# Kernel tuning notes

Measured on AMD Instinct MI355X. Metric: run time of the kernel, lower is better.

## Reference

```python
import jax, jax.numpy as jnp
import numpy as np

B, LQ, NK, D, H, FF, NL = 32, 96, 2048, 384, 8, 1536, 6
DH = D // H
NFUT = 32
GOAL_S, GRASP_S = 2046, 2047  # goal=[2046,2047), grasp=[2047,2048) in k_cross and k_self


def rotary3d(xyz):
    # RotaryPositionEncoding3D: per-axis sinusoids, interleaved duplication, concat over x/y/z
    d3 = D // 3
    div = jnp.exp(jnp.arange(0, d3, 2, dtype=jnp.float32) * (-np.log(10000.0) / d3))  # [d3/2]
    ang = xyz[..., None] * div  # [B,N,3,d3/2]
    cos = jnp.repeat(jnp.cos(ang), 2, axis=-1)  # [B,N,3,d3] (f0,f0,f1,f1,...)
    sin = jnp.repeat(jnp.sin(ang), 2, axis=-1)
    b, n = xyz.shape[:2]
    return cos.reshape(b, n, D), sin.reshape(b, n, D)


def rope(x, cos, sin):
    x2 = jnp.stack([-x[..., 1::2], x[..., ::2]], axis=-1).reshape(x.shape)
    return x * cos + x2 * sin


def layernorm(x, g, b):
    m = jnp.mean(x, -1, keepdims=True)
    v = jnp.var(x, -1, keepdims=True)
    return (x - m) * jax.lax.rsqrt(v + 1e-5) * g + b


def attn_block(x, kv, qcos, qsin, kcos, ksin, t_feats, p):
    (aw, ab, wq_, bq_, wk_, bk_, wv_, bv_, wo_, bo_, g1, b1, fw1_, fb1_, fw2_, fb2_, g2, b2_) = p
    # AdaLN: time-conditioned scale/shift on the query stream
    mod = jax.nn.silu(t_feats) @ aw + ab  # [B,2D]
    scale, shift = jnp.split(mod, 2, axis=-1)
    xq = x * (1.0 + scale[:, None, :]) + shift[:, None, :]
    qp = rope(xq @ wq_ + bq_, qcos, qsin).reshape(B, -1, H, DH)
    kp = rope(kv @ wk_ + bk_, kcos, ksin).reshape(B, -1, H, DH)
    vp = (kv @ wv_ + bv_).reshape(B, -1, H, DH)
    att = jax.nn.softmax(jnp.einsum('bqhd,bkhd->bhqk', qp, kp) / np.sqrt(DH), axis=-1)
    o = jnp.einsum('bhqk,bkhd->bqhd', att, vp).reshape(B, -1, D) @ wo_ + bo_
    x = layernorm(x + o, g1, b1)  # post-norm (pre_norm=False), residual on un-modulated x
    f = jax.nn.relu(x @ fw1_ + fb1_) @ fw2_ + fb2_
    return layernorm(x + f, g2, b2_)


def mlp_head(x, w1, b1, w2, b2, w3, b3):
    h = jax.nn.relu(x @ w1 + b1)
    h = jax.nn.relu(h @ w2 + b2)
    return h @ w3 + b3


def _forward(q, k_cross, k_self, q_xyz, k_xyz, timesteps,
             t_w1, t_b1, t_w2, t_b2, type_emb,
             ada_w, ada_b, wq, bq, wk, bk, wv, bv, wo, bo,
             ln1_g, ln1_b, fw1, fb1, fw2, fb2, ln2_g, ln2_b,
             act_w1, act_b1, act_w2, act_b2, act_w3, act_b3,
             qf_w1, qf_b1, qf_w2, qf_b2, qf_w3, qf_b3,
             ob_w1, ob_b1, ob_w2, ob_b2, ob_w3, ob_b3):
    # SinusoidalPosEmb + MLP time embedding
    half = D // 2
    freqs = jnp.exp(jnp.arange(half, dtype=jnp.float32) * (-np.log(10000.0) / (half - 1)))
    a = timesteps[:, None] * freqs
    pe = jnp.concatenate([jnp.sin(a), jnp.cos(a)], axis=-1)
    t_feats = jax.nn.relu(pe @ t_w1 + t_b1) @ t_w2 + t_b2  # [B,D]

    qcos, qsin = rotary3d(q_xyz)
    kcos, ksin = rotary3d(k_xyz)
    scos = jnp.concatenate([kcos, qcos], axis=1)  # self layers: seq2_pos = cat(pcd, grasp)
    ssin = jnp.concatenate([ksin, qsin], axis=1)

    # type embeddings (conditions_only -> goal=id3, grasp=id4)
    kc = k_cross.at[:, GOAL_S:GOAL_S + 1].add(type_emb[3]).at[:, GRASP_S:GRASP_S + 1].add(type_emb[4])
    ksf = k_self.at[:, GOAL_S:GOAL_S + 1].add(type_emb[3]).at[:, GRASP_S:GRASP_S + 1].add(type_emb[4])

    x = q
    for i in range(NL):
        p = (ada_w[i], ada_b[i], wq[i], bq[i], wk[i], bk[i], wv[i], bv[i], wo[i], bo[i],
             ln1_g[i], ln1_b[i], fw1[i], fb1[i], fw2[i], fb2[i], ln2_g[i], ln2_b[i])
        if i < 2:  # cross_attn module (2 layers) over scene tokens
            x = attn_block(x, kc, qcos, qsin, kcos, ksin, t_feats, p)
        else:      # 4 shared attention layers over k_self
            x = attn_block(x, ksf, qcos, qsin, scos, ssin, t_feats, p)

    act = mlp_head(x[:, :NFUT], act_w1, act_b1, act_w2, act_b2, act_w3, act_b3)            # [B,32,31]
    qf = mlp_head(x[:, NFUT:2 * NFUT], qf_w1, qf_b1, qf_w2, qf_b2, qf_w3, qf_b3)           # [B,32,31]
    ob = mlp_head(x[:, 2 * NFUT:], ob_w1, ob_b1, ob_w2, ob_b2, ob_w3, ob_b3)               # [B,32,9]
    return jnp.concatenate([act, qf, ob], axis=-1)  # [B,32,71]


def setup_inputs():
    ks = iter(jax.random.split(jax.random.key(0), 80))
    def w(shape, s=0.02):
        return jax.random.normal(next(ks), shape, jnp.float32) * s
    inp = {
        'q': jax.random.normal(next(ks), (B, LQ, D), jnp.float32),
        'k_cross': jax.random.normal(next(ks), (B, NK, D), jnp.float32),
        'k_self': jax.random.normal(next(ks), (B, NK + LQ, D), jnp.float32),
        'q_xyz': jax.random.normal(next(ks), (B, LQ, 3), jnp.float32),
        'k_xyz': jax.random.normal(next(ks), (B, NK, 3), jnp.float32),
        'timesteps': jax.random.uniform(next(ks), (B,), jnp.float32) * 1000.0,
        't_w1': w((D, D)), 't_b1': jnp.zeros((D,)), 't_w2': w((D, D)), 't_b2': jnp.zeros((D,)),
        'type_emb': w((8, D)),
        'ada_w': w((NL, D, 2 * D)), 'ada_b': jnp.zeros((NL, 2 * D)),
        'wq': w((NL, D, D)), 'bq': jnp.zeros((NL, D)),
        'wk': w((NL, D, D)), 'bk': jnp.zeros((NL, D)),
        'wv': w((NL, D, D)), 'bv': jnp.zeros((NL, D)),
        'wo': w((NL, D, D)), 'bo': jnp.zeros((NL, D)),
        'ln1_g': jnp.ones((NL, D)), 'ln1_b': jnp.zeros((NL, D)),
        'fw1': w((NL, D, FF)), 'fb1': jnp.zeros((NL, FF)),
        'fw2': w((NL, FF, D)), 'fb2': jnp.zeros((NL, D)),
        'ln2_g': jnp.ones((NL, D)), 'ln2_b': jnp.zeros((NL, D)),
        'act_w1': w((D, D)), 'act_b1': jnp.zeros((D,)), 'act_w2': w((D, D)), 'act_b2': jnp.zeros((D,)),
        'act_w3': w((D, 31)), 'act_b3': jnp.zeros((31,)),
        'qf_w1': w((D, D)), 'qf_b1': jnp.zeros((D,)), 'qf_w2': w((D, D)), 'qf_b2': jnp.zeros((D,)),
        'qf_w3': w((D, 31)), 'qf_b3': jnp.zeros((31,)),
        'ob_w1': w((D, D)), 'ob_b1': jnp.zeros((D,)), 'ob_w2': w((D, D)), 'ob_b2': jnp.zeros((D,)),
        'ob_w3': w((D, 9)), 'ob_b3': jnp.zeros((9,)),
    }
    return inp


def reference(q, k_cross, k_self, q_xyz, k_xyz, timesteps,
              t_w1, t_b1, t_w2, t_b2, type_emb,
              ada_w, ada_b, wq, bq, wk, bk, wv, bv, wo, bo,
              ln1_g, ln1_b, fw1, fb1, fw2, fb2, ln2_g, ln2_b,
              act_w1, act_b1, act_w2, act_b2, act_w3, act_b3,
              qf_w1, qf_b1, qf_w2, qf_b2, qf_w3, qf_b3,
              ob_w1, ob_b1, ob_w2, ob_b2, ob_w3, ob_b3):
    return _forward(q, k_cross, k_self, q_xyz, k_xyz, timesteps,
                    t_w1, t_b1, t_w2, t_b2, type_emb,
                    ada_w, ada_b, wq, bq, wk, bk, wv, bv, wo, bo,
                    ln1_g, ln1_b, fw1, fb1, fw2, fb2, ln2_g, ln2_b,
                    act_w1, act_b1, act_w2, act_b2, act_w3, act_b3,
                    qf_w1, qf_b1, qf_w2, qf_b2, qf_w3, qf_b3,
                    ob_w1, ob_b1, ob_w2, ob_b2, ob_w3, ob_b3)
```

## Files before the change

### kernel.cpp

```cpp
#include <hip/hip_runtime.h>
#include <hip/hip_fp16.h>

#define B_   32
#define LQ_  96
#define NK_  2048
#define D_   384
#define H_   8
#define DH_  48
#define FF_  1536
#define MQ_  (B_*LQ_)
#define SATT 8

typedef float  f32x4  __attribute__((ext_vector_type(4)));
typedef __bf16 bf16x8 __attribute__((ext_vector_type(8)));

__device__ __forceinline__ unsigned short f2bf(float f) {
  union { float f; unsigned u; } v; v.f = f;
  unsigned r = v.u + 0x7fffu + ((v.u >> 16) & 1u);
  return (unsigned short)(r >> 16);
}

__device__ __forceinline__ void ld_g2l(const unsigned short* g, unsigned short* l) {
  __builtin_amdgcn_global_load_lds(
      (const __attribute__((address_space(1))) void*)g,
      (__attribute__((address_space(3))) void*)l, 16, 0, 0);
}

__global__ void time_embed_kernel(const float* __restrict__ ts,
                                  const float* __restrict__ w1, const float* __restrict__ b1,
                                  const float* __restrict__ w2, const float* __restrict__ b2,
                                  float* __restrict__ s_out) {
  int b = blockIdx.x, d = threadIdx.x;
  __shared__ float pe[384];
  __shared__ float h1[384];
  float t = ts[b];
  int dd = (d < 192) ? d : d - 192;
  float f = expf((float)dd * (-9.210340371976184f / 191.0f));
  float ang = t * f;
  pe[d] = (d < 192) ? sinf(ang) : cosf(ang);
  __syncthreads();
  float acc = b1[d];
  for (int k = 0; k < 384; ++k) acc += pe[k] * w1[k * 384 + d];
  h1[d] = fmaxf(acc, 0.f);
  __syncthreads();
  acc = b2[d];
  for (int k = 0; k < 384; ++k) acc += h1[k] * w2[k * 384 + d];
  s_out[b * 384 + d] = acc / (1.f + expf(-acc));
}

__global__ void adaln_mod_kernel(const float* __restrict__ s,
                                 const float* __restrict__ aw, const float* __restrict__ ab,
                                 float* __restrict__ mod) {
  int b = blockIdx.x, l = blockIdx.y, c = threadIdx.x;
  __shared__ float ss[384];
  if (c < 384) ss[c] = s[b * 384 + c];
  __syncthreads();
  float acc = ab[l * 768 + c];
  const float* w = aw + (long)l * 384 * 768;
  for (int k = 0; k < 384; ++k) acc += ss[k] * w[k * 768 + c];
  mod[((long)l * 32 + b) * 768 + c] = acc;
}

__global__ void rope_pack_kernel(const float* __restrict__ xyz, __half2* __restrict__ cs,
                                 int total, int N, int ldn, int noff) {
  for (int i = blockIdx.x * blockDim.x + threadIdx.x; i < total;
       i += gridDim.x * blockDim.x) {
    int p = i % 192;
    int n = (i / 192) % N;
    int b = i / (192 * N);
    int a = p >> 6, j = p & 63;
    float div = __expf((float)j * (-9.210340371976184f / 64.0f));
    float ang = xyz[((long)b * N + n) * 3 + a] * div;
    float sv, cv;
    __sincosf(ang, &sv, &cv);
    cs[((long)b * ldn + noff + n) * 192 + p] = __floats2half2_rn(cv, sv);
  }
}

__global__ void cast_type_kernel(const float* __restrict__ in, const float* __restrict__ temb,
                                 unsigned short* __restrict__ out, long total, int N) {
  for (long i = blockIdx.x * (long)blockDim.x + threadIdx.x; i < total;
       i += (long)gridDim.x * blockDim.x) {
    int d = (int)(i % 384);
    int n = (int)((i / 384) % N);
    float v = in[i];
    if (n == 2046) v += temb[3 * 384 + d];
    else if (n == 2047) v += temb[4 * 384 + d];
    out[i] = f2bf(v);
  }
}

__global__ void wtrans_kernel(const float* __restrict__ in, unsigned short* __restrict__ out,
                              long total, int K, int N, int LDN, int noff) {
  for (long i = blockIdx.x * (long)blockDim.x + threadIdx.x; i < total;
       i += (long)gridDim.x * blockDim.x) {
    long l = i / ((long)K * N);
    long rem = i - l * (long)K * N;
    int n = (int)(rem / K);
    int k = (int)(rem % K);
    out[(l * LDN + noff + n) * K + k] = f2bf(in[l * (long)K * N + (long)k * N + n]);
  }
}

__global__ void modx_kernel(const float* __restrict__ x, const float* __restrict__ modl,
                            unsigned short* __restrict__ xq) {
  int i = blockIdx.x * blockDim.x + threadIdx.x;
  if (i >= MQ_ * D_) return;
  int d = i % 384;
  int b = (i / 384) / 96;
  float sc = modl[b * 768 + d];
  float sh = modl[b * 768 + 384 + d];
  xq[i] = f2bf(x[i] * (1.f + sc) + sh);
}

#define EPI_RELU   1
#define EPI_F32    2
#define EPI_ROPE_Q 3
#define EPI_KV     4

template <int EPI, int TM, int XT, int PERM>
__global__ __launch_bounds__(256)
void gemm_bt(const unsigned short* __restrict__ A, const unsigned short* __restrict__ Bt,
             const float* __restrict__ biasK, const float* __restrict__ biasV,
             void* __restrict__ Cout, void* __restrict__ Cout2,
             int Nt, int K, const __half2* __restrict__ cs, int tabOff, int nPerRow) {
  __shared__ __align__(16) unsigned short As[2][TM * 32];
  __shared__ __align__(16) unsigned short Bs[2][128 * 32];
  int tid = threadIdx.x, lane = tid & 63, wid = tid >> 6;
  int wm = (wid >> 1) * (TM / 2), wn = (wid & 1) * 64;
  int bx, byi;
  if (XT > 0) {
    int id = blockIdx.x;
    int xcd = id & 7, slot = id >> 3;
    bx = slot % XT;
    byi = (slot / XT) * 8 + xcd;
  } else {
    bx = blockIdx.x; byi = blockIdx.y;
  }
  int bn = bx * 128;
  long bm = (long)byi * TM;
  int r0 = tid >> 2;
  int cg = ((tid & 3) + (tid >> 3)) & 3;
  int c0 = cg * 8;
  long ar0 = bm + r0, ar1 = bm + 64 + r0;
  if (PERM) {
    ar0 = (ar0 >> 5) * 96 + tabOff + (ar0 & 31);
    ar1 = (ar1 >> 5) * 96 + tabOff + (ar1 & 31);
  }
  const unsigned short* gA0 = A + ar0 * K + c0;
  const unsigned short* gA1 = A + ar1 * K + c0;
  const unsigned short* gB0 = Bt + (long)(bn + r0) * K + c0;
  const unsigned short* gB1 = Bt + (long)(bn + 64 + r0) * K + c0;
  f32x4 acc[TM / 32][4] = {};
  int nk = K >> 5;
  int la = lane & 15, lg8 = lane >> 4;
  ld_g2l(gA0, &As[0][tid * 8]);
  if (TM == 128) ld_g2l(gA1, &As[0][2048 + tid * 8]);
  ld_g2l(gB0, &Bs[0][tid * 8]);
  ld_g2l(gB1, &Bs[0][2048 + tid * 8]);
  gA0 += 32; gA1 += 32; gB0 += 32; gB1 += 32;
  int offA[TM / 32], offB[4];
#pragma unroll
  for (int i = 0; i < TM / 32; ++i) {
    int row = wm + i * 16 + la;
    offA[i] = row * 32 + ((lg8 - (row >> 1)) & 3) * 8;
  }
#pragma unroll
  for (int j = 0; j < 4; ++j) {
    int row = wn + j * 16 + la;
    offB[j] = row * 32 + ((lg8 - (row >> 1)) & 3) * 8;
  }
  __syncthreads();
  for (int kc = 0; kc < nk; ++kc) {
    int cur = kc & 1;
    if (kc + 1 < nk) {
      int nxt = cur ^ 1;
      ld_g2l(gA0, &As[nxt][tid * 8]);
      if (TM == 128) ld_g2l(gA1, &As[nxt][2048 + tid * 8]);
      ld_g2l(gB0, &Bs[nxt][tid * 8]);
      ld_g2l(gB1, &Bs[nxt][2048 + tid * 8]);
      gA0 += 32; gA1 += 32; gB0 += 32; gB1 += 32;
    }
    bf16x8 af[TM / 32], bfr[4];
#pragma unroll
    for (int i = 0; i < TM / 32; ++i) af[i] = *(const bf16x8*)&As[cur][offA[i]];
#pragma unroll
    for (int j = 0; j < 4; ++j) bfr[j] = *(const bf16x8*)&Bs[cur][offB[j]];
#pragma unroll
    for (int i = 0; i < TM / 32; ++i)
#pragma unroll
      for (int j = 0; j < 4; ++j)
        acc[i][j] = __builtin_amdgcn_mfma_f32_16x16x32_bf16(af[i], bfr[j], acc[i][j], 0, 0, 0);
    __syncthreads();
  }
  int lr = lg8 * 4;
  const float SCALE = 0.14433756729740643f;
  bool isV = false;
  const float* bptr = biasK;
  if (EPI == EPI_KV) { isV = (bn >= 384); if (isV) bptr = biasV - 384; }
#pragma unroll
  for (int i = 0; i < TM / 32; ++i) {
#pragma unroll
    for (int r = 0; r < 4; ++r) {
      int row = (int)bm + wm + i * 16 + lr + r;
      int bb = 0, nn = 0; long ti = 0;
      if (EPI == EPI_ROPE_Q || EPI == EPI_KV) {
        bb = row / nPerRow;
        nn = row - bb * nPerRow;
        ti = ((long)bb * 2144 + tabOff + nn) * 192;
      }
#pragma unroll
      for (int j = 0; j < 4; ++j) {
        int col = bn + wn + j * 16 + la;
        float v = acc[i][j][r] + bptr[col];
        if (EPI == EPI_F32) {
          ((float*)Cout)[(long)row * Nt + col] = v;
        } else if (EPI == EPI_RELU) {
          ((unsigned short*)Cout)[(long)row * Nt + col] = f2bf(fmaxf(v, 0.f));
        } else if (EPI == EPI_KV && isV) {
          ((unsigned short*)Cout2)[(long)row * 384 + (col - 384)] = f2bf(v);
        } else {
          float pv = __shfl_xor(v, 1);
          int p = ((col >> 7) << 6) + ((col & 127) >> 1);
          __half2 hv = cs[ti + p];
          float cc = __low2float(hv), ssv = __high2float(hv);
          float o = (col & 1) ? (v * cc + pv * ssv) : (v * cc - pv * ssv);
          if (EPI == EPI_ROPE_Q) {
            ((unsigned short*)Cout)[(long)row * Nt + col] = f2bf(o * SCALE);
          } else {
            int h = col / 48, d = col - h * 48;
            ((unsigned short*)Cout)[((long)((bb << 3) + h) * nPerRow + nn) * 48 + d] = f2bf(o);
          }
        }
      }
    }
  }
}

__global__ __launch_bounds__(384)
void attn_part_kernel(const unsigned short* __restrict__ Q, const unsigned short* __restrict__ Kg,
                      const unsigned short* __restrict__ Vrm, float* __restrict__ Opart,
                      float* __restrict__ Lpart, int N, int S) {
  int h = blockIdx.x, b = blockIdx.y, s = blockIdx.z;
  int bh = b * 8 + h;
  int tid = threadIdx.x, lane = tid & 63, w = tid >> 6;
  __shared__ __align__(16) unsigned short Qs[96][64];
  __shared__ __align__(16) unsigned short Ks[32][72];
  __shared__ __align__(16) unsigned short Vst[64][40];
  __shared__ __align__(16) unsigned short Ps[6][16][40];
  const uint4 z4 = {0u, 0u, 0u, 0u};
  for (int e = tid; e < 576; e += 384) {
    int row = e / 6, g = e % 6;
    *(uint4*)&Qs[row][g * 8] = *(const uint4*)&Q[((long)b * 96 + row) * 384 + h * 48 + g * 8];
  }
  for (int e = tid; e < 192; e += 384) {
    int row = e >> 1, g = e & 1;
    *(uint4*)&Qs[row][48 + g * 8] = z4;
  }
  if (tid < 96) {
    int row = tid / 3, g = tid % 3;
    *(uint4*)&Ks[row][48 + g * 8] = z4;
  }
  if (tid < 75) *(uint4*)&Vst[49][0 + tid * 8] = z4;
  if (tid < 40) Vst[48][tid] = (tid < 32) ? (unsigned short)0x3F80 : (unsigned short)0;
  __syncthreads();
  int la = lane & 15, lg = (lane >> 4) * 8;
  bf16x8 qf0 = *(const bf16x8*)&Qs[w * 16 + la][lg];
  bf16x8 qf1 = *(const bf16x8*)&Qs[w * 16 + la][32 + lg];
  f32x4 of[4] = {};
  int ntile = N >> 5;
  int t0 = (s * ntile) / S, t1 = ((s + 1) * ntile) / S;
  int stt = (tid < 192) ? tid : tid - 192;
  int krow = stt / 6, kg = stt % 6;
  const uint4* gsrc = (tid < 192)
      ? (const uint4*)(Kg + ((long)bh * N + krow) * 48 + kg * 8)
      : (const uint4*)(Vrm + ((long)b * N + krow) * 384 + h * 48 + kg * 8);
  int tstep = (tid < 192) ? 192 : 1536;
  uint4 pref = gsrc[(long)t0 * tstep];
  for (int it = t0; it < t1; ++it) {
    if (tid < 192) {
      *(uint4*)&Ks[krow][kg * 8] = pref;
    } else {
      union { uint4 q; unsigned short u[8]; } t; t.q = pref;
#pragma unroll
      for (int e = 0; e < 8; ++e) Vst[kg * 8 + e][krow] = t.u[e];
    }
    __syncthreads();
    if (it + 1 < t1) pref = gsrc[(long)(it + 1) * tstep];
    f32x4 sc[2] = {};
#pragma unroll
    for (int ctile = 0; ctile < 2; ++ctile) {
      bf16x8 kf0 = *(const bf16x8*)&Ks[ctile * 16 + la][lg];
      bf16x8 kf1 = *(const bf16x8*)&Ks[ctile * 16 + la][32 + lg];
      sc[ctile] = __builtin_amdgcn_mfma_f32_16x16x32_bf16(qf0, kf0, sc[ctile], 0, 0, 0);
      sc[ctile] = __builtin_amdgcn_mfma_f32_16x16x32_bf16(qf1, kf1, sc[ctile], 0, 0, 0);
    }
    int prow = (lane >> 4) * 4;
#pragma unroll
    for (int ctile = 0; ctile < 2; ++ctile)
#pragma unroll
      for (int r = 0; r < 4; ++r)
        Ps[w][prow + r][ctile * 16 + la] = f2bf(__expf(sc[ctile][r]));
    __asm__ volatile("s_waitcnt lgkmcnt(0)" ::: "memory");
    bf16x8 pf = *(const bf16x8*)&Ps[w][la][lg];
#pragma unroll
    for (int dt = 0; dt < 4; ++dt) {
      bf16x8 vf = *(const bf16x8*)&Vst[dt * 16 + la][lg];
      of[dt] = __builtin_amdgcn_mfma_f32_16x16x32_bf16(pf, vf, of[dt], 0, 0, 0);
    }
    __syncthreads();
  }
  long base = ((long)s * 256 + bh) * 96;
#pragma unroll
  for (int r = 0; r < 4; ++r) {
    int qrow = w * 16 + (lane >> 4) * 4 + r;
    float L = __shfl(of[3][r], lane & 48);
#pragma unroll
    for (int dt = 0; dt < 3; ++dt)
      Opart[(base + qrow) * 48 + dt * 16 + la] = of[dt][r];
    if (la == 0) Lpart[base + qrow] = L;
  }
}

__global__ __launch_bounds__(384)
void attn_combine_kernel(const float* __restrict__ Opart, const float* __restrict__ Lpart,
                         unsigned short* __restrict__ O, int S) {
  int h = blockIdx.x, b = blockIdx.y;
  int bh = b * 8 + h;
  for (int e = threadIdx.x; e < 96 * 48; e += 384) {
    int q = e / 48, d = e % 48;
    float L = 0.f, acc = 0.f;
    for (int s = 0; s < S; ++s) {
      long ib = ((long)s * 256 + bh) * 96 + q;
      L += Lpart[ib];
      acc += Opart[ib * 48 + d];
    }
    O[((long)b * 96 + q) * 384 + h * 48 + d] = f2bf(acc / L);
  }
}

__global__ __launch_bounds__(128)
void ln_res_kernel(const float* __restrict__ xin, const float* __restrict__ delta,
                   const float* __restrict__ g, const float* __restrict__ bt,
                   const float* __restrict__ modl,
                   float* __restrict__ xout, unsigned short* __restrict__ xbf,
                   unsigned short* __restrict__ xqb) {
  int row = blockIdx.x, tid = threadIdx.x;
  __shared__ float red[128];
  float v[3];
#pragma unroll
  for (int i = 0; i < 3; ++i) {
    int d = tid + i * 128;
    v[i] = xin[(long)row * 384 + d] + delta[(long)row * 384 + d];
  }
  red[tid] = v[0] + v[1] + v[2];
  __syncthreads();
  for (int t = 64; t > 0; t >>= 1) { if (tid < t) red[tid] += red[tid + t]; __syncthreads(); }
  float mean = red[0] / 384.f;
  __syncthreads();
  float q = 0.f;
#pragma unroll
  for (int i = 0; i < 3; ++i) { float d0 = v[i] - mean; q += d0 * d0; }
  red[tid] = q;
  __syncthreads();
  for (int t = 64; t > 0; t >>= 1) { if (tid < t) red[tid] += red[tid + t]; __syncthreads(); }
  float rstd = rsqrtf(red[0] / 384.f + 1e-5f);
  int bb = row / 96;
#pragma unroll
  for (int i = 0; i < 3; ++i) {
    int d = tid + i * 128;
    float o = (v[i] - mean) * rstd * g[d] + bt[d];
    xout[(long)row * 384 + d] = o;
    xbf[(long)row * 384 + d] = f2bf(o);
    if (modl) {
      float sc = modl[bb * 768 + d];
      float sh = modl[bb * 768 + 384 + d];
      xqb[(long)row * 384 + d] = f2bf(o * (1.f + sc) + sh);
    }
  }
}

__global__ __launch_bounds__(64)
void rowgemm_bf(const unsigned short* __restrict__ A, const float* __restrict__ W,
                const float* __restrict__ bias, float* __restrict__ out,
                int Nc, int ooff) {
  int r = blockIdx.x, tid = threadIdx.x;
  __shared__ float as[384];
  for (int k = tid; k < 384; k += 64) {
    union { unsigned u; float f; } c; c.u = (unsigned)A[(long)r * 384 + k] << 16;
    as[k] = c.f;
  }
  __syncthreads();
  if (tid < Nc) {
    float acc = bias[tid];
    for (int k = 0; k < 384; ++k) acc += as[k] * W[k * Nc + tid];
    out[(long)r * 71 + ooff + tid] = acc;
  }
}

extern "C" void kernel_launch(void* const* d_in, const int* in_sizes, int n_in,
                              void* d_out, int out_size, void* d_ws, size_t ws_size,
                              hipStream_t stream) {
  const float* q_in    = (const float*)d_in[0];
  const float* k_cross = (const float*)d_in[1];
  const float* k_self  = (const float*)d_in[2];
  const float* q_xyz   = (const float*)d_in[3];
  const float* k_xyz   = (const float*)d_in[4];
  const float* tsteps  = (const float*)d_in[5];
  const float* t_w1 = (const float*)d_in[6];
  const float* t_b1 = (const float*)d_in[7];
  const float* t_w2 = (const float*)d_in[8];
  const float* t_b2 = (const float*)d_in[9];
  const float* type_emb = (const float*)d_in[10];
  const float* ada_w = (const float*)d_in[11];
  const float* ada_b = (const float*)d_in[12];
  const float* wq = (const float*)d_in[13]; const float* bq = (const float*)d_in[14];
  const float* wk = (const float*)d_in[15]; const float* bk = (const float*)d_in[16];
  const float* wv = (const float*)d_in[17]; const float* bv = (const float*)d_in[18];
  const float* wo = (const float*)d_in[19]; const float* bo = (const float*)d_in[20];
  const float* ln1g = (const float*)d_in[21]; const float* ln1b = (const float*)d_in[22];
  const float* fw1 = (const float*)d_in[23]; const float* fb1 = (const float*)d_in[24];
  const float* fw2 = (const float*)d_in[25]; const float* fb2 = (const float*)d_in[26];
  const float* ln2g = (const float*)d_in[27]; const float* ln2b = (const float*)d_in[28];
  const float* hw[9]; const float* hb[9];
  for (int i = 0; i < 9; ++i) { hw[i] = (const float*)d_in[29 + 2 * i]; hb[i] = (const float*)d_in[30 + 2 * i]; }

  char* ws = (char*)d_ws;
  size_t off = 0;
  auto alloc = [&](size_t bytes) -> void* {
    void* p = ws + off;
    off += (bytes + 255) & ~(size_t)255;
    return p;
  };
  float* s_silu = (float*)alloc((size_t)32 * 384 * 4);
  float* mod    = (float*)alloc((size_t)6 * 32 * 768 * 4);
  __half2* cs_all = (__half2*)alloc((size_t)32 * 2144 * 192 * 4);
  unsigned short* kcb  = (unsigned short*)alloc((size_t)32 * 2048 * 384 * 2);
  unsigned short* ksb  = (unsigned short*)alloc((size_t)32 * 2144 * 384 * 2);
  unsigned short* wqt  = (unsigned short*)alloc((size_t)6 * 384 * 384 * 2);
  unsigned short* wkvt = (unsigned short*)alloc((size_t)6 * 768 * 384 * 2);
  unsigned short* wot  = (unsigned short*)alloc((size_t)6 * 384 * 384 * 2);
  unsigned short* fw1t = (unsigned short*)alloc((size_t)6 * 384 * 1536 * 2);
  unsigned short* fw2t = (unsigned short*)alloc((size_t)6 * 384 * 1536 * 2);
  unsigned short* hwt  = (unsigned short*)alloc((size_t)6 * 384 * 384 * 2);
  float* x            = (float*)alloc((size_t)MQ_ * 384 * 4);
  unsigned short* xbf  = (unsigned short*)alloc((size_t)MQ_ * 384 * 2);
  unsigned short* xqb  = (unsigned short*)alloc((size_t)MQ_ * 384 * 2);
  unsigned short* qrope= (unsigned short*)alloc((size_t)MQ_ * 384 * 2);
  unsigned short* Kc   = (unsigned short*)alloc((size_t)256 * 2144 * 48 * 2);
  unsigned short* Vrm  = (unsigned short*)alloc((size_t)32 * 2144 * 384 * 2);
  unsigned short* aout = (unsigned short*)alloc((size_t)MQ_ * 384 * 2);
  float* tmp          = (float*)alloc((size_t)MQ_ * 384 * 4);
  unsigned short* ffh  = (unsigned short*)alloc((size_t)MQ_ * 1536 * 2);
  unsigned short* hh1  = (unsigned short*)alloc((size_t)1024 * 384 * 2);
  unsigned short* hh2  = (unsigned short*)alloc((size_t)1024 * 384 * 2);
  float* Opart        = (float*)alloc((size_t)SATT * 256 * 96 * 48 * 4);
  float* Lpart        = (float*)alloc((size_t)SATT * 256 * 96 * 4);
  (void)ws_size; (void)in_sizes; (void)n_in; (void)out_size;

  time_embed_kernel<<<32, 384, 0, stream>>>(tsteps, t_w1, t_b1, t_w2, t_b2, s_silu);
  adaln_mod_kernel<<<dim3(32, 6), 768, 0, stream>>>(s_silu, ada_w, ada_b, mod);
  rope_pack_kernel<<<4096, 256, 0, stream>>>(k_xyz, cs_all, 32 * 2048 * 192, 2048, 2144, 0);
  rope_pack_kernel<<<1024, 256, 0, stream>>>(q_xyz, cs_all, 32 * 96 * 192, 96, 2144, 2048);
  cast_type_kernel<<<4096, 256, 0, stream>>>(k_cross, type_emb, kcb, (long)32 * 2048 * 384, 2048);
  cast_type_kernel<<<4096, 256, 0, stream>>>(k_self, type_emb, ksb, (long)32 * 2144 * 384, 2144);
  wtrans_kernel<<<1024, 256, 0, stream>>>(wq, wqt, (long)6 * 384 * 384, 384, 384, 384, 0);
  wtrans_kernel<<<1024, 256, 0, stream>>>(wk, wkvt, (long)6 * 384 * 384, 384, 384, 768, 0);
  wtrans_kernel<<<1024, 256, 0, stream>>>(wv, wkvt, (long)6 * 384 * 384, 384, 384, 768, 384);
  wtrans_kernel<<<1024, 256, 0, stream>>>(wo, wot, (long)6 * 384 * 384, 384, 384, 384, 0);
  wtrans_kernel<<<2048, 256, 0, stream>>>(fw1, fw1t, (long)6 * 384 * 1536, 384, 1536, 1536, 0);
  wtrans_kernel<<<2048, 256, 0, stream>>>(fw2, fw2t, (long)6 * 1536 * 384, 1536, 384, 384, 0);
  for (int hd = 0; hd < 3; ++hd) {
    wtrans_kernel<<<256, 256, 0, stream>>>(hw[hd * 3 + 0], hwt + (long)(hd * 2) * 384 * 384,
                                           (long)384 * 384, 384, 384, 384, 0);
    wtrans_kernel<<<256, 256, 0, stream>>>(hw[hd * 3 + 1], hwt + (long)(hd * 2 + 1) * 384 * 384,
                                           (long)384 * 384, 384, 384, 384, 0);
  }
  hipMemcpyAsync(x, q_in, (size_t)MQ_ * 384 * 4, hipMemcpyDeviceToDevice, stream);
  modx_kernel<<<(MQ_ * 384 + 255) / 256, 256, 0, stream>>>(x, mod, xqb);

  for (int l = 0; l < 6; ++l) {
    int Nl = (l < 2) ? 2048 : 2144;
    const unsigned short* kvsrc = (l < 2) ? kcb : ksb;
    gemm_bt<EPI_ROPE_Q, 64, 0, 0><<<dim3(3, 48), 256, 0, stream>>>(
        xqb, wqt + (long)l * 384 * 384, bq + l * 384, nullptr, qrope, nullptr,
        384, 384, cs_all, 2048, 96);
    gemm_bt<EPI_KV, 128, 6, 0><<<dim3(6 * (32 * Nl / 128)), 256, 0, stream>>>(
        kvsrc, wkvt + (long)l * 768 * 384, bk + l * 384, bv + l * 384, Kc, Vrm,
        768, 384, cs_all, 0, Nl);
    attn_part_kernel<<<dim3(8, 32, SATT), 384, 0, stream>>>(qrope, Kc, Vrm, Opart, Lpart, Nl, SATT);
    attn_combine_kernel<<<dim3(8, 32), 384, 0, stream>>>(Opart, Lpart, aout, SATT);
    gemm_bt<EPI_F32, 64, 0, 0><<<dim3(3, 48), 256, 0, stream>>>(
        aout, wot + (long)l * 384 * 384, bo + l * 384, nullptr, tmp, nullptr,
        384, 384, nullptr, 0, 96);
    ln_res_kernel<<<MQ_, 128, 0, stream>>>(x, tmp, ln1g + l * 384, ln1b + l * 384,
                                           nullptr, x, xbf, nullptr);
    gemm_bt<EPI_RELU, 128, 0, 0><<<dim3(12, 24), 256, 0, stream>>>(
        xbf, fw1t + (long)l * 1536 * 384, fb1 + l * 1536, nullptr, ffh, nullptr,
        1536, 384, nullptr, 0, 96);
    gemm_bt<EPI_F32, 64, 0, 0><<<dim3(3, 48), 256, 0, stream>>>(
        ffh, fw2t + (long)l * 384 * 1536, fb2 + l * 384, nullptr, tmp, nullptr,
        384, 1536, nullptr, 0, 96);
    ln_res_kernel<<<MQ_, 128, 0, stream>>>(x, tmp, ln2g + l * 384, ln2b + l * 384,
                                           (l < 5) ? (mod + (long)(l + 1) * 32 * 768) : nullptr,
                                           x, xbf, xqb);
  }

  const int ooffs[3] = {0, 31, 62};
  const int nouts[3] = {31, 31, 9};
  for (int hd = 0; hd < 3; ++hd) {
    gemm_bt<EPI_RELU, 64, 0, 1><<<dim3(3, 16), 256, 0, stream>>>(
        xbf, hwt + (long)(hd * 2) * 384 * 384, hb[hd * 3 + 0], nullptr, hh1, nullptr,
        384, 384, nullptr, hd * 32, 96);
    gemm_bt<EPI_RELU, 64, 0, 0><<<dim3(3, 16), 256, 0, stream>>>(
        hh1, hwt + (long)(hd * 2 + 1) * 384 * 384, hb[hd * 3 + 1], nullptr, hh2, nullptr,
        384, 384, nullptr, 0, 96);
    rowgemm_bf<<<1024, 64, 0, stream>>>(hh2, hw[hd * 3 + 2], hb[hd * 3 + 2], (float*)d_out,
                                        nouts[hd], ooffs[hd]);
  }
}
```

Before: 2.351 ms.

## Triple-buffer GEMM LDS staging and double-buffer attention K/V tiles with one barrier

The GEMM moves from double to triple LDS buffering, with loads issued two tiles ahead. Each iteration now uses a single barrier guarded by explicit vmcnt/lgkmcnt waits instead of two __syncthreads. The attention kernel double-buffers its K and V shared tiles, which removes the trailing barrier per key tile, and it rotates the V-transpose store order to cut LDS bank conflicts. This aims to hide more global latency and synchronization cost, at the price of extra LDS per block, which can lower occupancy, and correctness that now depends on the hand-counted waitcnt values.

```diff
diff --git a/kernel.cpp b/kernel.cpp
--- a/kernel.cpp
+++ b/kernel.cpp
@@ -124,8 +124,8 @@
              const float* __restrict__ biasK, const float* __restrict__ biasV,
              void* __restrict__ Cout, void* __restrict__ Cout2,
              int Nt, int K, const __half2* __restrict__ cs, int tabOff, int nPerRow) {
-  __shared__ __align__(16) unsigned short As[2][TM * 32];
-  __shared__ __align__(16) unsigned short Bs[2][128 * 32];
+  __shared__ __align__(16) unsigned short As[3][TM * 32];
+  __shared__ __align__(16) unsigned short Bs[3][128 * 32];
   int tid = threadIdx.x, lane = tid & 63, wid = tid >> 6;
   int wm = (wid >> 1) * (TM / 2), wn = (wid & 1) * 64;
   int bx, byi;
@@ -154,11 +154,13 @@
   f32x4 acc[TM / 32][4] = {};
   int nk = K >> 5;
   int la = lane & 15, lg8 = lane >> 4;
-  ld_g2l(gA0, &As[0][tid * 8]);
-  if (TM == 128) ld_g2l(gA1, &As[0][2048 + tid * 8]);
-  ld_g2l(gB0, &Bs[0][tid * 8]);
-  ld_g2l(gB1, &Bs[0][2048 + tid * 8]);
-  gA0 += 32; gA1 += 32; gB0 += 32; gB1 += 32;
+  auto stage = [&](int buf) {
+    ld_g2l(gA0, &As[buf][tid * 8]);
+    if (TM == 128) ld_g2l(gA1, &As[buf][2048 + tid * 8]);
+    ld_g2l(gB0, &Bs[buf][tid * 8]);
+    ld_g2l(gB1, &Bs[buf][2048 + tid * 8]);
+    gA0 += 32; gA1 += 32; gB0 += 32; gB1 += 32;
+  };
   int offA[TM / 32], offB[4];
 #pragma unroll
   for (int i = 0; i < TM / 32; ++i) {
@@ -170,28 +172,30 @@
     int row = wn + j * 16 + la;
     offB[j] = row * 32 + ((lg8 - (row >> 1)) & 3) * 8;
   }
-  __syncthreads();
+  stage(0);
+  stage(1);
   for (int kc = 0; kc < nk; ++kc) {
-    int cur = kc & 1;
-    if (kc + 1 < nk) {
-      int nxt = cur ^ 1;
-      ld_g2l(gA0, &As[nxt][tid * 8]);
-      if (TM == 128) ld_g2l(gA1, &As[nxt][2048 + tid * 8]);
-      ld_g2l(gB0, &Bs[nxt][tid * 8]);
-      ld_g2l(gB1, &Bs[nxt][2048 + tid * 8]);
-      gA0 += 32; gA1 += 32; gB0 += 32; gB1 += 32;
-    }
+    int cur = kc % 3;
+    if (kc < nk - 1) {
+      if (TM == 128) asm volatile("s_waitcnt vmcnt(4) lgkmcnt(0)" ::: "memory");
+      else           asm volatile("s_waitcnt vmcnt(3) lgkmcnt(0)" ::: "memory");
+    } else {
+      asm volatile("s_waitcnt vmcnt(0) lgkmcnt(0)" ::: "memory");
+    }
+    asm volatile("s_barrier" ::: "memory");
+    if (kc + 2 < nk) stage((kc + 2) % 3);
+    const unsigned short* Ab = &As[cur][0];
+    const unsigned short* Bb = &Bs[cur][0];
     bf16x8 af[TM / 32], bfr[4];
 #pragma unroll
-    for (int i = 0; i < TM / 32; ++i) af[i] = *(const bf16x8*)&As[cur][offA[i]];
-#pragma unroll
-    for (int j = 0; j < 4; ++j) bfr[j] = *(const bf16x8*)&Bs[cur][offB[j]];
+    for (int i = 0; i < TM / 32; ++i) af[i] = *(const bf16x8*)&Ab[offA[i]];
+#pragma unroll
+    for (int j = 0; j < 4; ++j) bfr[j] = *(const bf16x8*)&Bb[offB[j]];
 #pragma unroll
     for (int i = 0; i < TM / 32; ++i)
 #pragma unroll
       for (int j = 0; j < 4; ++j)
         acc[i][j] = __builtin_amdgcn_mfma_f32_16x16x32_bf16(af[i], bfr[j], acc[i][j], 0, 0, 0);
-    __syncthreads();
   }
   int lr = lg8 * 4;
   const float SCALE = 0.14433756729740643f;
@@ -245,8 +249,8 @@
   int bh = b * 8 + h;
   int tid = threadIdx.x, lane = tid & 63, w = tid >> 6;
   __shared__ __align__(16) unsigned short Qs[96][64];
-  __shared__ __align__(16) unsigned short Ks[32][72];
-  __shared__ __align__(16) unsigned short Vst[64][40];
+  __shared__ __align__(16) unsigned short Ks[2][32][72];
+  __shared__ __align__(16) unsigned short Vst[2][64][40];
   __shared__ __align__(16) unsigned short Ps[6][16][40];
   const uint4 z4 = {0u, 0u, 0u, 0u};
   for (int e = tid; e < 576; e += 384) {
@@ -257,12 +261,18 @@
     int row = e >> 1, g = e & 1;
     *(uint4*)&Qs[row][48 + g * 8] = z4;
   }
-  if (tid < 96) {
-    int row = tid / 3, g = tid % 3;
-    *(uint4*)&Ks[row][48 + g * 8] = z4;
-  }
-  if (tid < 75) *(uint4*)&Vst[49][0 + tid * 8] = z4;
-  if (tid < 40) Vst[48][tid] = (tid < 32) ? (unsigned short)0x3F80 : (unsigned short)0;
+  if (tid < 192) {
+    int pb = tid / 96, rr = (tid % 96) / 3, g = tid % 3;
+    *(uint4*)&Ks[pb][rr][48 + g * 8] = z4;
+  }
+  if (tid < 150) {
+    int pb = tid / 75, e = tid % 75;
+    *(uint4*)(&Vst[pb][49][0] + e * 8) = z4;
+  }
+  if (tid < 80) {
+    int pb = tid / 40, c = tid % 40;
+    Vst[pb][48][c] = (c < 32) ? (unsigned short)0x3F80 : (unsigned short)0;
+  }
   __syncthreads();
   int la = lane & 15, lg = (lane >> 4) * 8;
   bf16x8 qf0 = *(const bf16x8*)&Qs[w * 16 + la][lg];
@@ -278,20 +288,25 @@
   int tstep = (tid < 192) ? 192 : 1536;
   uint4 pref = gsrc[(long)t0 * tstep];
   for (int it = t0; it < t1; ++it) {
+    int p = it & 1;
     if (tid < 192) {
-      *(uint4*)&Ks[krow][kg * 8] = pref;
+      *(uint4*)&Ks[p][krow][kg * 8] = pref;
     } else {
       union { uint4 q; unsigned short u[8]; } t; t.q = pref;
 #pragma unroll
-      for (int e = 0; e < 8; ++e) Vst[kg * 8 + e][krow] = t.u[e];
-    }
-    __syncthreads();
+      for (int e = 0; e < 8; ++e) {
+        int ee = (e + kg) & 7;
+        Vst[p][kg * 8 + ee][krow] = t.u[ee];
+      }
+    }
+    asm volatile("s_waitcnt lgkmcnt(0)" ::: "memory");
+    asm volatile("s_barrier" ::: "memory");
     if (it + 1 < t1) pref = gsrc[(long)(it + 1) * tstep];
     f32x4 sc[2] = {};
 #pragma unroll
     for (int ctile = 0; ctile < 2; ++ctile) {
-      bf16x8 kf0 = *(const bf16x8*)&Ks[ctile * 16 + la][lg];
-      bf16x8 kf1 = *(const bf16x8*)&Ks[ctile * 16 + la][32 + lg];
+      bf16x8 kf0 = *(const bf16x8*)&Ks[p][ctile * 16 + la][lg];
+      bf16x8 kf1 = *(const bf16x8*)&Ks[p][ctile * 16 + la][32 + lg];
       sc[ctile] = __builtin_amdgcn_mfma_f32_16x16x32_bf16(qf0, kf0, sc[ctile], 0, 0, 0);
       sc[ctile] = __builtin_amdgcn_mfma_f32_16x16x32_bf16(qf1, kf1, sc[ctile], 0, 0, 0);
     }
@@ -301,14 +316,13 @@
 #pragma unroll
       for (int r = 0; r < 4; ++r)
         Ps[w][prow + r][ctile * 16 + la] = f2bf(__expf(sc[ctile][r]));
-    __asm__ volatile("s_waitcnt lgkmcnt(0)" ::: "memory");
+    asm volatile("s_waitcnt lgkmcnt(0)" ::: "memory");
     bf16x8 pf = *(const bf16x8*)&Ps[w][la][lg];
 #pragma unroll
     for (int dt = 0; dt < 4; ++dt) {
-      bf16x8 vf = *(const bf16x8*)&Vst[dt * 16 + la][lg];
+      bf16x8 vf = *(const bf16x8*)&Vst[p][dt * 16 + la][lg];
       of[dt] = __builtin_amdgcn_mfma_f32_16x16x32_bf16(pf, vf, of[dt], 0, 0, 0);
     }
-    __syncthreads();
   }
   long base = ((long)s * 256 + bh) * 96;
 #pragma unroll
```

Measured after the change: 2.426 ms. 3.2% more time.
